# Optimization experiments

Hardware: AMD Instinct MI355X
Metric: run time of the kernel (lower is better)

Reference implementation:

```python
import jax, jax.numpy as jnp
import numpy as np

N_NODES = 50000


def _gine(x, src, dst, edge_embed, lin_w, lin_b, nn_w, nn_b):
    # PyG GINEConv (eps=0): out = nn(x + sum_{j->i} ReLU(x_j + lin(edge_attr)))
    e = edge_embed @ lin_w + lin_b              # [E, d_in]
    msg = jax.nn.relu(x[src] + e)               # gather + fuse, [E, d_in]
    agg = jax.ops.segment_sum(msg, dst, num_segments=N_NODES)  # scatter-add, [N, d_in]
    return (x + agg) @ nn_w + nn_b              # small MLP, [N, d_out]


def setup_inputs() -> dict:
    key = jax.random.key(0)
    ks = jax.random.split(key, 20)
    E = 800000
    h = 128
    sc = lambda f_in: 1.0 / np.sqrt(f_in)
    inp = {
        "x": jax.random.normal(ks[0], (N_NODES, 1), jnp.float32),
        "edge_index": jax.random.randint(ks[1], (2, E), 0, N_NODES, jnp.int64),
        "edge_attr": jax.random.normal(ks[2], (E, 1), jnp.float32),
        "em_w": jax.random.normal(ks[3], (1, h), jnp.float32) * sc(1),
        "em_b": jnp.zeros((h,), jnp.float32),
        "l1_w": jax.random.normal(ks[4], (h, 1), jnp.float32) * sc(h),
        "l1_b": jnp.zeros((1,), jnp.float32),
        "n1_w": jax.random.normal(ks[5], (1, h), jnp.float32) * sc(1),
        "n1_b": jnp.zeros((h,), jnp.float32),
        "l2_w": jax.random.normal(ks[6], (h, h), jnp.float32) * sc(h),
        "l2_b": jnp.zeros((h,), jnp.float32),
        "n2_w": jax.random.normal(ks[7], (h, h), jnp.float32) * sc(h),
        "n2_b": jnp.zeros((h,), jnp.float32),
        "l3_w": jax.random.normal(ks[8], (h, h), jnp.float32) * sc(h),
        "l3_b": jnp.zeros((h,), jnp.float32),
        "n3_w": jax.random.normal(ks[9], (h, h), jnp.float32) * sc(h),
        "n3_b": jnp.zeros((h,), jnp.float32),
        "dec_w": jax.random.normal(ks[10], (2 * h, 1), jnp.float32) * sc(2 * h),
        "dec_b": jnp.zeros((1,), jnp.float32),
    }
    return inp


def reference(x, edge_index, edge_attr, em_w, em_b, l1_w, l1_b, n1_w, n1_b,
              l2_w, l2_b, n2_w, n2_b, l3_w, l3_b, n3_w, n3_b, dec_w, dec_b):
    src, dst = edge_index[0], edge_index[1]
    edge_embed = edge_attr @ em_w + em_b                      # [E, 128]
    hdn = _gine(x,   src, dst, edge_embed, l1_w, l1_b, n1_w, n1_b)
    hdn = _gine(hdn, src, dst, edge_embed, l2_w, l2_b, n2_w, n2_b)
    hdn = _gine(hdn, src, dst, edge_embed, l3_w, l3_b, n3_w, n3_b)
    h_cat = jnp.concatenate([hdn[src], hdn[dst]], axis=-1)    # [E, 256]
    return h_cat @ dec_w + dec_b                              # [E, 1]
```

## Files before the change

kernel.cpp:

```cpp
#include <hip/hip_runtime.h>

#define H 128
#define CAPC 5376


typedef unsigned long long ull;
using bf16x8 = __attribute__((ext_vector_type(8))) short;
using f32x4  = __attribute__((ext_vector_type(4))) float;

__device__ __forceinline__ float bf2f(unsigned short v) {
  return __uint_as_float(((unsigned)v) << 16);
}
__device__ __forceinline__ unsigned short bf16r(float v) {
  unsigned u = __float_as_uint(v);
  u = (u + 0x7FFFu + ((u >> 16) & 1u)) >> 16;
  return (unsigned short)u;
}
__device__ __forceinline__ unsigned bf16pair(float a, float b) {
  return (unsigned)bf16r(a) | ((unsigned)bf16r(b) << 16);
}

__global__ __launch_bounds__(256) void init_consts(
    const float* __restrict__ em_w, const float* __restrict__ em_b,
    const float* __restrict__ l1_w, const float* __restrict__ l1_b,
    const float* __restrict__ l2_w, const float* __restrict__ l2_b,
    const float* __restrict__ n1_b,
    const float* __restrict__ l3_w, const float* __restrict__ l3_b,
    const float* __restrict__ n2w, const float* __restrict__ n3w,
    float* __restrict__ consts, int* __restrict__ cursor,
    unsigned short* __restrict__ w2t, unsigned short* __restrict__ w3t,
    int NBUCK) {
  if (blockIdx.x > 0) {
    const int i = (blockIdx.x - 1) * 256 + threadIdx.x;
    if (i < H * H) {
      const int j = i >> 7, k = i & (H - 1);
      w2t[k * H + j] = bf16r(n2w[i]);
    } else {
      const int ii = i - H * H;
      const int j = ii >> 7, k = ii & (H - 1);
      w3t[k * H + j] = bf16r(n3w[ii]);
    }
    return;
  }
  const int k = threadIdx.x;
  if (k < NBUCK) cursor[k] = 0;
  __shared__ float sa[H], sc[H];
  if (k < H) {
    float u2 = 0.f, c2 = 0.f, u3 = 0.f, c3 = 0.f;
    for (int j = 0; j < H; ++j) {
      const float ew = em_w[j], eb = em_b[j];
      u2 = fmaf(ew, l2_w[j * H + k], u2);
      c2 = fmaf(eb, l2_w[j * H + k], c2);
      u3 = fmaf(ew, l3_w[j * H + k], u3);
      c3 = fmaf(eb, l3_w[j * H + k], c3);
    }
    consts[2 + k]         = u2;
    consts[2 + H + k]     = c2 + l2_b[k] + n1_b[k];
    consts[2 + 2 * H + k] = u3;
    consts[2 + 3 * H + k] = c3 + l3_b[k];
    sa[k] = em_w[k] * l1_w[k];
    sc[k] = em_b[k] * l1_w[k];
  }
  __syncthreads();
  for (int s = 64; s > 0; s >>= 1) {
    if (k < s) { sa[k] += sa[k + s]; sc[k] += sc[k + s]; }
    __syncthreads();
  }
  if (k == 0) { consts[0] = sa[0]; consts[1] = sc[0] + l1_b[0]; }
}

__global__ __launch_bounds__(1024) void bin_scatter(
    const int* __restrict__ src, const int* __restrict__ dst,
    const float* __restrict__ ea, int* __restrict__ cursor,
    ull* __restrict__ spc, int E, int NBUCK) {
  __shared__ int lhist[256];
  __shared__ int lbase[256];
  const int tid = threadIdx.x;
  const int base = blockIdx.x * 2048 + tid * 2;
  if (tid < 256) lhist[tid] = 0;
  __syncthreads();
  int s_[2], d_[2], b_[2], r_[2];
  float a_[2];
#pragma unroll
  for (int j = 0; j < 2; ++j) {
    const int e = base + j;
    if (e < E) {
      s_[j] = src[e]; d_[j] = dst[e]; a_[j] = ea[e];
      b_[j] = d_[j] >> 8;
      r_[j] = atomicAdd(&lhist[b_[j]], 1);
    } else {
      b_[j] = -1;
    }
  }
  __syncthreads();
  if (tid < NBUCK && lhist[tid] > 0)
    lbase[tid] = atomicAdd(&cursor[tid], lhist[tid]);
  __syncthreads();
#pragma unroll
  for (int j = 0; j < 2; ++j) {
    if (b_[j] >= 0) {
      const int pl = lbase[b_[j]] + r_[j];
      if (pl < CAPC)
        spc[(size_t)b_[j] * CAPC + pl] =
            ((ull)(unsigned)(s_[j] | ((d_[j] & 255) << 16)) << 32) |
            (ull)(unsigned)__float_as_uint(a_[j]);
    }
  }
}

__global__ __launch_bounds__(1024) void fine_scatter(
    const int* __restrict__ cursor, const ull* __restrict__ spc,
    const float* __restrict__ x, const float* __restrict__ consts,
    int2* __restrict__ spf, int* __restrict__ rowstart,
    float* __restrict__ s1, int N) {
  __shared__ int lh[256];
  __shared__ int sd[256];
  __shared__ int cur[256];
  __shared__ int2 pay[CAPC];
  const int tid = threadIdx.x;
  const int b = blockIdx.x;
  const int cnt = min(cursor[b], CAPC);
  const size_t rbase = (size_t)b * CAPC;
  if (tid < 256) lh[tid] = 0;
  __syncthreads();
  for (int i = tid; i < cnt; i += 1024)
    atomicAdd(&lh[(int)((spc[rbase + i] >> 48) & 255u)], 1);
  __syncthreads();
  if (tid < 256) sd[tid] = lh[tid];
  __syncthreads();
  for (int off = 1; off < 256; off <<= 1) {
    int t = 0;
    if (tid < 256 && tid >= off) t = sd[tid - off];
    __syncthreads();
    if (tid < 256) sd[tid] += t;
    __syncthreads();
  }
  if (tid < 256) {
    const int ex = sd[tid] - lh[tid];
    cur[tid] = ex;
    rowstart[b * 257 + tid] = (int)rbase + ex;
    if (tid == 0) rowstart[b * 257 + 256] = (int)rbase + cnt;
  }
  __syncthreads();
  for (int i = tid; i < cnt; i += 1024) {
    const ull payv = spc[rbase + i];
    const int dl = (int)((payv >> 48) & 255u);
    const int pos = atomicAdd(&cur[dl], 1);
    pay[pos] = make_int2((int)((payv >> 32) & 0xFFFFu), (int)(unsigned)payv);
  }
  __syncthreads();
  for (int i = tid; i < cnt; i += 1024) spf[rbase + i] = pay[i];
  const int lane = tid & 63, wid = tid >> 6;
  const float a1 = consts[0], c1 = consts[1];
  for (int i = wid; i < 256; i += 16) {
    const int n = (b << 8) + i;
    if (n >= N) break;
    const int rsl = sd[i] - lh[i], ci = lh[i];
    float part = 0.f;
    for (int j = lane; j < ci; j += 64) {
      const int2 pv = pay[rsl + j];
      part += fmaxf(x[pv.x] + fmaf(a1, __int_as_float(pv.y), c1), 0.f);
    }
#pragma unroll
    for (int o = 32; o >= 1; o >>= 1) part += __shfl_xor(part, o, 64);
    if (lane == 0) s1[n] = x[n] + part;
  }
}

__global__ __launch_bounds__(256) void edge2_csr(
    const int* __restrict__ rowstart, const int2* __restrict__ sp,
    const float* __restrict__ s1, const float* __restrict__ n1w,
    const float* __restrict__ n1b, const float* __restrict__ consts,
    unsigned short* __restrict__ t2b, int N) {
  const int n = (blockIdx.x * blockDim.x + threadIdx.x) >> 6;
  const int lane = threadIdx.x & 63;
  if (n >= N) return;
  const int rbase = (n >> 8) * 257 + (n & 255);
  const int rs = rowstart[rbase], re = rowstart[rbase + 1];
  const float w0 = n1w[lane],            w1 = n1w[lane + 64];
  const float u0 = consts[2 + lane],     u1 = consts[2 + lane + 64];
  const float c0 = consts[2 + H + lane], c1 = consts[2 + H + lane + 64];
  float acc0 = 0.f, acc1 = 0.f;
  for (int base = rs; base < re; base += 64) {
    const int i = base + lane;
    float s1v = 0.f, eav = 0.f;
    if (i < re) {
      const int2 sv = sp[i];
      s1v = s1[sv.x];
      eav = __int_as_float(sv.y);
    }
    const int cnt = min(64, re - base);
    for (int j = 0; j < cnt; ++j) {
      const float s = __shfl(s1v, j, 64);
      const float a = __shfl(eav, j, 64);
      acc0 += fmaxf(fmaf(s, w0, fmaf(a, u0, c0)), 0.f);
      acc1 += fmaxf(fmaf(s, w1, fmaf(a, u1, c1)), 0.f);
    }
  }
  const float sn = s1[n];
  t2b[(size_t)n * H + lane]      = bf16r(fmaf(sn, w0, n1b[lane])      + acc0);
  t2b[(size_t)n * H + lane + 64] = bf16r(fmaf(sn, w1, n1b[lane + 64]) + acc1);
}

__global__ __launch_bounds__(256) void edge3_csr(
    const int* __restrict__ rowstart, const int2* __restrict__ sp,
    const unsigned short* __restrict__ h2b, const float* __restrict__ consts,
    unsigned short* __restrict__ t3b, int N) {
  const int n = (blockIdx.x * blockDim.x + threadIdx.x) >> 6;
  const int lane = threadIdx.x & 63;
  if (n >= N) return;
  const int rbase = (n >> 8) * 257 + (n & 255);
  const int rs = rowstart[rbase], re = rowstart[rbase + 1];
  const int k0 = 2 * lane;
  const float u0 = consts[2 + 2 * H + k0], u1 = consts[2 + 2 * H + k0 + 1];
  const float c0 = consts[2 + 3 * H + k0], c1 = consts[2 + 3 * H + k0 + 1];
  float acc0 = 0.f, acc1 = 0.f;
  int i = rs;
  for (; i + 4 <= re; i += 4) {
    const int2 e0 = sp[i], e1 = sp[i + 1], e2 = sp[i + 2], e3 = sp[i + 3];
    const ushort2 h0 = *(const ushort2*)&h2b[(size_t)e0.x * H + k0];
    const ushort2 h1 = *(const ushort2*)&h2b[(size_t)e1.x * H + k0];
    const ushort2 h2v = *(const ushort2*)&h2b[(size_t)e2.x * H + k0];
    const ushort2 h3 = *(const ushort2*)&h2b[(size_t)e3.x * H + k0];
    const float a0 = __int_as_float(e0.y), a1 = __int_as_float(e1.y);
    const float a2 = __int_as_float(e2.y), a3 = __int_as_float(e3.y);
    acc0 += fmaxf(bf2f(h0.x) + fmaf(a0, u0, c0), 0.f);
    acc1 += fmaxf(bf2f(h0.y) + fmaf(a0, u1, c1), 0.f);
    acc0 += fmaxf(bf2f(h1.x) + fmaf(a1, u0, c0), 0.f);
    acc1 += fmaxf(bf2f(h1.y) + fmaf(a1, u1, c1), 0.f);
    acc0 += fmaxf(bf2f(h2v.x) + fmaf(a2, u0, c0), 0.f);
    acc1 += fmaxf(bf2f(h2v.y) + fmaf(a2, u1, c1), 0.f);
    acc0 += fmaxf(bf2f(h3.x) + fmaf(a3, u0, c0), 0.f);
    acc1 += fmaxf(bf2f(h3.y) + fmaf(a3, u1, c1), 0.f);
  }
  for (; i < re; ++i) {
    const int2 ev = sp[i];
    const ushort2 hv = *(const ushort2*)&h2b[(size_t)ev.x * H + k0];
    const float a = __int_as_float(ev.y);
    acc0 += fmaxf(bf2f(hv.x) + fmaf(a, u0, c0), 0.f);
    acc1 += fmaxf(bf2f(hv.y) + fmaf(a, u1, c1), 0.f);
  }
  const ushort2 hn = *(const ushort2*)&h2b[(size_t)n * H + k0];
  ((unsigned*)t3b)[(size_t)n * 64 + lane] =
      bf16pair(bf2f(hn.x) + acc0, bf2f(hn.y) + acc1);
}

__global__ __launch_bounds__(256) void mlp2_mfma(
    const unsigned short* __restrict__ t2b, unsigned short* __restrict__ h2b,
    const unsigned short* __restrict__ w2t, const float* __restrict__ n2b,
    int N) {
  __shared__ unsigned short dt[4][16 * H];
  const int tid = threadIdx.x, w = tid >> 6, lane = tid & 63;
  const int col = lane & 15, quad = lane >> 4;
  const int tile = blockIdx.x * 4 + w;
  const int node0 = tile * 16;
  const bf16x8* arow =
      (const bf16x8*)(t2b + (size_t)(node0 + col) * H + quad * 8);
  const bf16x8 a0 = arow[0], a1 = arow[4], a2 = arow[8], a3 = arow[12];
#pragma unroll
  for (int t = 0; t < 8; ++t) {
    const bf16x8* bcol =
        (const bf16x8*)(w2t + (size_t)(t * 16 + col) * H + quad * 8);
    f32x4 acc = {0.f, 0.f, 0.f, 0.f};
    acc = __builtin_amdgcn_mfma_f32_16x16x32_bf16(a0, bcol[0], acc, 0, 0, 0);
    acc = __builtin_amdgcn_mfma_f32_16x16x32_bf16(a1, bcol[4], acc, 0, 0, 0);
    acc = __builtin_amdgcn_mfma_f32_16x16x32_bf16(a2, bcol[8], acc, 0, 0, 0);
    acc = __builtin_amdgcn_mfma_f32_16x16x32_bf16(a3, bcol[12], acc, 0, 0, 0);
    const float bias = n2b[t * 16 + col];
#pragma unroll
    for (int r = 0; r < 4; ++r)
      dt[w][(quad * 4 + r) * H + t * 16 + col] = bf16r(acc[r] + bias);
  }
  __syncthreads();
  const unsigned* du = (const unsigned*)dt;
  unsigned* gu = (unsigned*)h2b;
  const int nb = blockIdx.x * 64;
  for (int i = tid; i < 64 * 64; i += 256) {
    const int r = i >> 6;
    if (nb + r < N) gu[(size_t)(nb + r) * 64 + (i & 63)] = du[i];
  }
}

__global__ __launch_bounds__(256) void mlp3_mfma(
    const unsigned short* __restrict__ t3b, const unsigned short* __restrict__ w3t,
    const float* __restrict__ n3b, const float* __restrict__ dec_w,
    float* __restrict__ p, float* __restrict__ q, int N) {
  __shared__ float dt3[4][16 * H];
  const int tid = threadIdx.x, w = tid >> 6, lane = tid & 63;
  const int col = lane & 15, quad = lane >> 4;
  const int tile = blockIdx.x * 4 + w;
  const int node0 = tile * 16;
  const bf16x8* arow =
      (const bf16x8*)(t3b + (size_t)(node0 + col) * H + quad * 8);
  const bf16x8 a0 = arow[0], a1 = arow[4], a2 = arow[8], a3 = arow[12];
#pragma unroll
  for (int t = 0; t < 8; ++t) {
    const bf16x8* bcol =
        (const bf16x8*)(w3t + (size_t)(t * 16 + col) * H + quad * 8);
    f32x4 acc = {0.f, 0.f, 0.f, 0.f};
    acc = __builtin_amdgcn_mfma_f32_16x16x32_bf16(a0, bcol[0], acc, 0, 0, 0);
    acc = __builtin_amdgcn_mfma_f32_16x16x32_bf16(a1, bcol[4], acc, 0, 0, 0);
    acc = __builtin_amdgcn_mfma_f32_16x16x32_bf16(a2, bcol[8], acc, 0, 0, 0);
    acc = __builtin_amdgcn_mfma_f32_16x16x32_bf16(a3, bcol[12], acc, 0, 0, 0);
    const float bias = n3b[t * 16 + col];
#pragma unroll
    for (int r = 0; r < 4; ++r)
      dt3[w][(quad * 4 + r) * H + t * 16 + col] = acc[r] + bias;
  }
  __syncthreads();
  const float dwA0 = dec_w[lane], dwA1 = dec_w[64 + lane];
  const float dwB0 = dec_w[128 + lane], dwB1 = dec_w[192 + lane];
#pragma unroll 4
  for (int r = 0; r < 16; ++r) {
    const float h0 = dt3[w][r * H + lane];
    const float h1 = dt3[w][r * H + 64 + lane];
    float pd = h0 * dwA0 + h1 * dwA1;
    float qd = h0 * dwB0 + h1 * dwB1;
#pragma unroll
    for (int o = 32; o >= 1; o >>= 1) {
      pd += __shfl_xor(pd, o, 64);
      qd += __shfl_xor(qd, o, 64);
    }
    const int n = node0 + r;
    if (lane == 0 && n < N) { p[n] = pd; q[n] = qd; }
  }
}

__global__ void final_kernel(const int* __restrict__ src,
                             const int* __restrict__ dst,
                             const float* __restrict__ p,
                             const float* __restrict__ q,
                             const float* __restrict__ dec_b,
                             float* __restrict__ out, int E) {
  const int e = blockIdx.x * blockDim.x + threadIdx.x;
  if (e < E) out[e] = p[src[e]] + q[dst[e]] + dec_b[0];
}

extern "C" void kernel_launch(void* const* d_in, const int* in_sizes, int n_in,
                              void* d_out, int out_size, void* d_ws, size_t ws_size,
                              hipStream_t stream) {
  const float* x     = (const float*)d_in[0];
  const int*   ei    = (const int*)d_in[1];
  const float* ea    = (const float*)d_in[2];
  const float* em_w  = (const float*)d_in[3];
  const float* em_b  = (const float*)d_in[4];
  const float* l1_w  = (const float*)d_in[5];
  const float* l1_b  = (const float*)d_in[6];
  const float* n1_w  = (const float*)d_in[7];
  const float* n1_b  = (const float*)d_in[8];
  const float* l2_w  = (const float*)d_in[9];
  const float* l2_b  = (const float*)d_in[10];
  const float* n2_w  = (const float*)d_in[11];
  const float* n2_b  = (const float*)d_in[12];
  const float* l3_w  = (const float*)d_in[13];
  const float* l3_b  = (const float*)d_in[14];
  const float* n3_w  = (const float*)d_in[15];
  const float* n3_b  = (const float*)d_in[16];
  const float* dec_w = (const float*)d_in[17];
  const float* dec_b = (const float*)d_in[18];
  float* out = (float*)d_out;

  const int N = in_sizes[0];
  const int E = in_sizes[2];
  const int* src = ei;
  const int* dst = ei + E;

  const int NBUCK  = (N + 255) >> 8;
  const int NBATCH = (E + 2047) >> 11;
  const int NPAD   = ((N + 63) / 64) * 64;
  const int NBLK64 = NPAD / 64;

  float* ws       = (float*)d_ws;
  float* consts   = ws;
  ull*   spc      = (ull*)(ws + 1024);
  int2*  spf      = (int2*)(spc + (size_t)NBUCK * CAPC);
  unsigned short* t2b = (unsigned short*)(spf + (size_t)NBUCK * CAPC);
  unsigned short* t3b = t2b + (size_t)NPAD * H;
  unsigned short* h2b = t3b + (size_t)NPAD * H;
  unsigned short* w2t = h2b + (size_t)NPAD * H;
  unsigned short* w3t = w2t + H * H;
  float* s1       = (float*)(w3t + H * H);
  float* p        = s1 + N;
  float* q        = p + N;
  int*   cursor   = (int*)(q + N);
  int*   rowstart = cursor + 256;

  init_consts<<<129, 256, 0, stream>>>(em_w, em_b, l1_w, l1_b, l2_w, l2_b,
                                       n1_b, l3_w, l3_b, n2_w, n3_w,
                                       consts, cursor, w2t, w3t, NBUCK);
  bin_scatter<<<NBATCH, 1024, 0, stream>>>(src, dst, ea, cursor, spc, E, NBUCK);
  fine_scatter<<<NBUCK, 1024, 0, stream>>>(cursor, spc, x, consts, spf,
                                           rowstart, s1, N);

  const int nwblocks = (N + 3) / 4;
  edge2_csr<<<nwblocks, 256, 0, stream>>>(rowstart, spf, s1, n1_w, n1_b,
                                          consts, t2b, N);
  mlp2_mfma<<<NBLK64, 256, 0, stream>>>(t2b, h2b, w2t, n2_b, N);
  edge3_csr<<<nwblocks, 256, 0, stream>>>(rowstart, spf, h2b, consts, t3b, N);
  mlp3_mfma<<<NBLK64, 256, 0, stream>>>(t3b, w3t, n3_b, dec_w, p, q, N);
  final_kernel<<<(E + 255) / 256, 256, 0, stream>>>(src, dst, p, q, dec_b, out, E);
}
```

Before: 246.7 us.

## Fuse all stages into one persistent cooperative kernel with grid syncs

Replaces the eight separate kernel launches with a single cooperative kernel whose phases are separated by grid-wide syncs, using a shared-memory union across phases and grid-stride loops. It also folds the decoder dot product directly into the layer-3 MFMA epilogue via shuffles, dropping the shared staging buffer, and processes four edges per thread in the binning phase. This removes launch gaps and tail effects between stages. In exchange, occupancy is capped by the large shared-memory union and the grid size, and each phase runs on a fixed grid of at most 512 blocks.

```diff
diff --git a/kernel.cpp b/kernel.cpp
--- a/kernel.cpp
+++ b/kernel.cpp
@@ -1,4 +1,5 @@
 #include <hip/hip_runtime.h>
+#include <hip/hip_cooperative_groups.h>
 
 #define H 128
 #define CAPC 5376
@@ -7,6 +8,7 @@
 typedef unsigned long long ull;
 using bf16x8 = __attribute__((ext_vector_type(8))) short;
 using f32x4  = __attribute__((ext_vector_type(4))) float;
+namespace cg = cooperative_groups;
 
 __device__ __forceinline__ float bf2f(unsigned short v) {
   return __uint_as_float(((unsigned)v) << 16);
@@ -20,383 +22,357 @@
   return (unsigned)bf16r(a) | ((unsigned)bf16r(b) << 16);
 }
 
-__global__ __launch_bounds__(256) void init_consts(
-    const float* __restrict__ em_w, const float* __restrict__ em_b,
-    const float* __restrict__ l1_w, const float* __restrict__ l1_b,
-    const float* __restrict__ l2_w, const float* __restrict__ l2_b,
-    const float* __restrict__ n1_b,
-    const float* __restrict__ l3_w, const float* __restrict__ l3_b,
-    const float* __restrict__ n2w, const float* __restrict__ n3w,
-    float* __restrict__ consts, int* __restrict__ cursor,
-    unsigned short* __restrict__ w2t, unsigned short* __restrict__ w3t,
-    int NBUCK) {
-  if (blockIdx.x > 0) {
-    const int i = (blockIdx.x - 1) * 256 + threadIdx.x;
+struct Params {
+  const float* x; const int* src; const int* dst; const float* ea;
+  const float *em_w, *em_b, *l1_w, *l1_b, *n1_w, *n1_b, *l2_w, *l2_b,
+              *n2_w, *n2_b, *l3_w, *l3_b, *n3_w, *n3_b, *dec_w, *dec_b;
+  float* consts; ull* spc; int2* spf;
+  unsigned short *t2b, *t3b, *h2b, *w2t, *w3t;
+  float *s1, *p, *q; int *cursor, *rowstart;
+  float* out;
+  int N, E, NBUCK, NBATCH, NT16;
+};
+
+__global__ __launch_bounds__(512, 4) void fused_kernel(Params P) {
+  cg::grid_group grid = cg::this_grid();
+  __shared__ union {
+    struct { float sa[H]; float sc[H]; } c0;
+    struct { int lhist[256]; int lbase[256]; } bin;
+    struct { int lh[256]; int sd[256]; int cur[256]; int2 pay[CAPC]; } fine;
+    struct { unsigned short dt[8][16 * H]; } m2;
+  } sm;
+  const int tid = threadIdx.x;
+  const int lane = tid & 63, w = tid >> 6;
+  const int GS = gridDim.x;
+
+  for (int i = blockIdx.x * 512 + tid; i < 2 * H * H; i += GS * 512) {
     if (i < H * H) {
       const int j = i >> 7, k = i & (H - 1);
-      w2t[k * H + j] = bf16r(n2w[i]);
+      P.w2t[k * H + j] = bf16r(P.n2_w[i]);
     } else {
       const int ii = i - H * H;
       const int j = ii >> 7, k = ii & (H - 1);
-      w3t[k * H + j] = bf16r(n3w[ii]);
-    }
-    return;
-  }
-  const int k = threadIdx.x;
-  if (k < NBUCK) cursor[k] = 0;
-  __shared__ float sa[H], sc[H];
-  if (k < H) {
-    float u2 = 0.f, c2 = 0.f, u3 = 0.f, c3 = 0.f;
-    for (int j = 0; j < H; ++j) {
-      const float ew = em_w[j], eb = em_b[j];
-      u2 = fmaf(ew, l2_w[j * H + k], u2);
-      c2 = fmaf(eb, l2_w[j * H + k], c2);
-      u3 = fmaf(ew, l3_w[j * H + k], u3);
-      c3 = fmaf(eb, l3_w[j * H + k], c3);
-    }
-    consts[2 + k]         = u2;
-    consts[2 + H + k]     = c2 + l2_b[k] + n1_b[k];
-    consts[2 + 2 * H + k] = u3;
-    consts[2 + 3 * H + k] = c3 + l3_b[k];
-    sa[k] = em_w[k] * l1_w[k];
-    sc[k] = em_b[k] * l1_w[k];
-  }
-  __syncthreads();
-  for (int s = 64; s > 0; s >>= 1) {
-    if (k < s) { sa[k] += sa[k + s]; sc[k] += sc[k + s]; }
-    __syncthreads();
-  }
-  if (k == 0) { consts[0] = sa[0]; consts[1] = sc[0] + l1_b[0]; }
-}
-
-__global__ __launch_bounds__(1024) void bin_scatter(
-    const int* __restrict__ src, const int* __restrict__ dst,
-    const float* __restrict__ ea, int* __restrict__ cursor,
-    ull* __restrict__ spc, int E, int NBUCK) {
-  __shared__ int lhist[256];
-  __shared__ int lbase[256];
-  const int tid = threadIdx.x;
-  const int base = blockIdx.x * 2048 + tid * 2;
-  if (tid < 256) lhist[tid] = 0;
-  __syncthreads();
-  int s_[2], d_[2], b_[2], r_[2];
-  float a_[2];
-#pragma unroll
-  for (int j = 0; j < 2; ++j) {
-    const int e = base + j;
-    if (e < E) {
-      s_[j] = src[e]; d_[j] = dst[e]; a_[j] = ea[e];
-      b_[j] = d_[j] >> 8;
-      r_[j] = atomicAdd(&lhist[b_[j]], 1);
-    } else {
-      b_[j] = -1;
-    }
-  }
-  __syncthreads();
-  if (tid < NBUCK && lhist[tid] > 0)
-    lbase[tid] = atomicAdd(&cursor[tid], lhist[tid]);
-  __syncthreads();
-#pragma unroll
-  for (int j = 0; j < 2; ++j) {
-    if (b_[j] >= 0) {
-      const int pl = lbase[b_[j]] + r_[j];
-      if (pl < CAPC)
-        spc[(size_t)b_[j] * CAPC + pl] =
-            ((ull)(unsigned)(s_[j] | ((d_[j] & 255) << 16)) << 32) |
-            (ull)(unsigned)__float_as_uint(a_[j]);
-    }
-  }
-}
-
-__global__ __launch_bounds__(1024) void fine_scatter(
-    const int* __restrict__ cursor, const ull* __restrict__ spc,
-    const float* __restrict__ x, const float* __restrict__ consts,
-    int2* __restrict__ spf, int* __restrict__ rowstart,
-    float* __restrict__ s1, int N) {
-  __shared__ int lh[256];
-  __shared__ int sd[256];
-  __shared__ int cur[256];
-  __shared__ int2 pay[CAPC];
-  const int tid = threadIdx.x;
-  const int b = blockIdx.x;
-  const int cnt = min(cursor[b], CAPC);
-  const size_t rbase = (size_t)b * CAPC;
-  if (tid < 256) lh[tid] = 0;
-  __syncthreads();
-  for (int i = tid; i < cnt; i += 1024)
-    atomicAdd(&lh[(int)((spc[rbase + i] >> 48) & 255u)], 1);
-  __syncthreads();
-  if (tid < 256) sd[tid] = lh[tid];
-  __syncthreads();
-  for (int off = 1; off < 256; off <<= 1) {
-    int t = 0;
-    if (tid < 256 && tid >= off) t = sd[tid - off];
-    __syncthreads();
-    if (tid < 256) sd[tid] += t;
-    __syncthreads();
-  }
-  if (tid < 256) {
-    const int ex = sd[tid] - lh[tid];
-    cur[tid] = ex;
-    rowstart[b * 257 + tid] = (int)rbase + ex;
-    if (tid == 0) rowstart[b * 257 + 256] = (int)rbase + cnt;
-  }
-  __syncthreads();
-  for (int i = tid; i < cnt; i += 1024) {
-    const ull payv = spc[rbase + i];
-    const int dl = (int)((payv >> 48) & 255u);
-    const int pos = atomicAdd(&cur[dl], 1);
-    pay[pos] = make_int2((int)((payv >> 32) & 0xFFFFu), (int)(unsigned)payv);
-  }
-  __syncthreads();
-  for (int i = tid; i < cnt; i += 1024) spf[rbase + i] = pay[i];
-  const int lane = tid & 63, wid = tid >> 6;
-  const float a1 = consts[0], c1 = consts[1];
-  for (int i = wid; i < 256; i += 16) {
-    const int n = (b << 8) + i;
-    if (n >= N) break;
-    const int rsl = sd[i] - lh[i], ci = lh[i];
-    float part = 0.f;
-    for (int j = lane; j < ci; j += 64) {
-      const int2 pv = pay[rsl + j];
-      part += fmaxf(x[pv.x] + fmaf(a1, __int_as_float(pv.y), c1), 0.f);
-    }
-#pragma unroll
-    for (int o = 32; o >= 1; o >>= 1) part += __shfl_xor(part, o, 64);
-    if (lane == 0) s1[n] = x[n] + part;
-  }
-}
-
-__global__ __launch_bounds__(256) void edge2_csr(
-    const int* __restrict__ rowstart, const int2* __restrict__ sp,
-    const float* __restrict__ s1, const float* __restrict__ n1w,
-    const float* __restrict__ n1b, const float* __restrict__ consts,
-    unsigned short* __restrict__ t2b, int N) {
-  const int n = (blockIdx.x * blockDim.x + threadIdx.x) >> 6;
-  const int lane = threadIdx.x & 63;
-  if (n >= N) return;
-  const int rbase = (n >> 8) * 257 + (n & 255);
-  const int rs = rowstart[rbase], re = rowstart[rbase + 1];
-  const float w0 = n1w[lane],            w1 = n1w[lane + 64];
-  const float u0 = consts[2 + lane],     u1 = consts[2 + lane + 64];
-  const float c0 = consts[2 + H + lane], c1 = consts[2 + H + lane + 64];
-  float acc0 = 0.f, acc1 = 0.f;
-  for (int base = rs; base < re; base += 64) {
-    const int i = base + lane;
-    float s1v = 0.f, eav = 0.f;
-    if (i < re) {
-      const int2 sv = sp[i];
-      s1v = s1[sv.x];
-      eav = __int_as_float(sv.y);
-    }
-    const int cnt = min(64, re - base);
-    for (int j = 0; j < cnt; ++j) {
-      const float s = __shfl(s1v, j, 64);
-      const float a = __shfl(eav, j, 64);
-      acc0 += fmaxf(fmaf(s, w0, fmaf(a, u0, c0)), 0.f);
-      acc1 += fmaxf(fmaf(s, w1, fmaf(a, u1, c1)), 0.f);
-    }
-  }
-  const float sn = s1[n];
-  t2b[(size_t)n * H + lane]      = bf16r(fmaf(sn, w0, n1b[lane])      + acc0);
-  t2b[(size_t)n * H + lane + 64] = bf16r(fmaf(sn, w1, n1b[lane + 64]) + acc1);
-}
-
-__global__ __launch_bounds__(256) void edge3_csr(
-    const int* __restrict__ rowstart, const int2* __restrict__ sp,
-    const unsigned short* __restrict__ h2b, const float* __restrict__ consts,
-    unsigned short* __restrict__ t3b, int N) {
-  const int n = (blockIdx.x * blockDim.x + threadIdx.x) >> 6;
-  const int lane = threadIdx.x & 63;
-  if (n >= N) return;
-  const int rbase = (n >> 8) * 257 + (n & 255);
-  const int rs = rowstart[rbase], re = rowstart[rbase + 1];
-  const int k0 = 2 * lane;
-  const float u0 = consts[2 + 2 * H + k0], u1 = consts[2 + 2 * H + k0 + 1];
-  const float c0 = consts[2 + 3 * H + k0], c1 = consts[2 + 3 * H + k0 + 1];
-  float acc0 = 0.f, acc1 = 0.f;
-  int i = rs;
-  for (; i + 4 <= re; i += 4) {
-    const int2 e0 = sp[i], e1 = sp[i + 1], e2 = sp[i + 2], e3 = sp[i + 3];
-    const ushort2 h0 = *(const ushort2*)&h2b[(size_t)e0.x * H + k0];
-    const ushort2 h1 = *(const ushort2*)&h2b[(size_t)e1.x * H + k0];
-    const ushort2 h2v = *(const ushort2*)&h2b[(size_t)e2.x * H + k0];
-    const ushort2 h3 = *(const ushort2*)&h2b[(size_t)e3.x * H + k0];
-    const float a0 = __int_as_float(e0.y), a1 = __int_as_float(e1.y);
-    const float a2 = __int_as_float(e2.y), a3 = __int_as_float(e3.y);
-    acc0 += fmaxf(bf2f(h0.x) + fmaf(a0, u0, c0), 0.f);
-    acc1 += fmaxf(bf2f(h0.y) + fmaf(a0, u1, c1), 0.f);
-    acc0 += fmaxf(bf2f(h1.x) + fmaf(a1, u0, c0), 0.f);
-    acc1 += fmaxf(bf2f(h1.y) + fmaf(a1, u1, c1), 0.f);
-    acc0 += fmaxf(bf2f(h2v.x) + fmaf(a2, u0, c0), 0.f);
-    acc1 += fmaxf(bf2f(h2v.y) + fmaf(a2, u1, c1), 0.f);
-    acc0 += fmaxf(bf2f(h3.x) + fmaf(a3, u0, c0), 0.f);
-    acc1 += fmaxf(bf2f(h3.y) + fmaf(a3, u1, c1), 0.f);
-  }
-  for (; i < re; ++i) {
-    const int2 ev = sp[i];
-    const ushort2 hv = *(const ushort2*)&h2b[(size_t)ev.x * H + k0];
-    const float a = __int_as_float(ev.y);
-    acc0 += fmaxf(bf2f(hv.x) + fmaf(a, u0, c0), 0.f);
-    acc1 += fmaxf(bf2f(hv.y) + fmaf(a, u1, c1), 0.f);
-  }
-  const ushort2 hn = *(const ushort2*)&h2b[(size_t)n * H + k0];
-  ((unsigned*)t3b)[(size_t)n * 64 + lane] =
-      bf16pair(bf2f(hn.x) + acc0, bf2f(hn.y) + acc1);
-}
-
-__global__ __launch_bounds__(256) void mlp2_mfma(
-    const unsigned short* __restrict__ t2b, unsigned short* __restrict__ h2b,
-    const unsigned short* __restrict__ w2t, const float* __restrict__ n2b,
-    int N) {
-  __shared__ unsigned short dt[4][16 * H];
-  const int tid = threadIdx.x, w = tid >> 6, lane = tid & 63;
-  const int col = lane & 15, quad = lane >> 4;
-  const int tile = blockIdx.x * 4 + w;
-  const int node0 = tile * 16;
-  const bf16x8* arow =
-      (const bf16x8*)(t2b + (size_t)(node0 + col) * H + quad * 8);
-  const bf16x8 a0 = arow[0], a1 = arow[4], a2 = arow[8], a3 = arow[12];
-#pragma unroll
-  for (int t = 0; t < 8; ++t) {
-    const bf16x8* bcol =
-        (const bf16x8*)(w2t + (size_t)(t * 16 + col) * H + quad * 8);
-    f32x4 acc = {0.f, 0.f, 0.f, 0.f};
-    acc = __builtin_amdgcn_mfma_f32_16x16x32_bf16(a0, bcol[0], acc, 0, 0, 0);
-    acc = __builtin_amdgcn_mfma_f32_16x16x32_bf16(a1, bcol[4], acc, 0, 0, 0);
-    acc = __builtin_amdgcn_mfma_f32_16x16x32_bf16(a2, bcol[8], acc, 0, 0, 0);
-    acc = __builtin_amdgcn_mfma_f32_16x16x32_bf16(a3, bcol[12], acc, 0, 0, 0);
-    const float bias = n2b[t * 16 + col];
-#pragma unroll
-    for (int r = 0; r < 4; ++r)
-      dt[w][(quad * 4 + r) * H + t * 16 + col] = bf16r(acc[r] + bias);
-  }
-  __syncthreads();
-  const unsigned* du = (const unsigned*)dt;
-  unsigned* gu = (unsigned*)h2b;
-  const int nb = blockIdx.x * 64;
-  for (int i = tid; i < 64 * 64; i += 256) {
-    const int r = i >> 6;
-    if (nb + r < N) gu[(size_t)(nb + r) * 64 + (i & 63)] = du[i];
-  }
-}
-
-__global__ __launch_bounds__(256) void mlp3_mfma(
-    const unsigned short* __restrict__ t3b, const unsigned short* __restrict__ w3t,
-    const float* __restrict__ n3b, const float* __restrict__ dec_w,
-    float* __restrict__ p, float* __restrict__ q, int N) {
-  __shared__ float dt3[4][16 * H];
-  const int tid = threadIdx.x, w = tid >> 6, lane = tid & 63;
-  const int col = lane & 15, quad = lane >> 4;
-  const int tile = blockIdx.x * 4 + w;
-  const int node0 = tile * 16;
-  const bf16x8* arow =
-      (const bf16x8*)(t3b + (size_t)(node0 + col) * H + quad * 8);
-  const bf16x8 a0 = arow[0], a1 = arow[4], a2 = arow[8], a3 = arow[12];
-#pragma unroll
-  for (int t = 0; t < 8; ++t) {
-    const bf16x8* bcol =
-        (const bf16x8*)(w3t + (size_t)(t * 16 + col) * H + quad * 8);
-    f32x4 acc = {0.f, 0.f, 0.f, 0.f};
-    acc = __builtin_amdgcn_mfma_f32_16x16x32_bf16(a0, bcol[0], acc, 0, 0, 0);
-    acc = __builtin_amdgcn_mfma_f32_16x16x32_bf16(a1, bcol[4], acc, 0, 0, 0);
-    acc = __builtin_amdgcn_mfma_f32_16x16x32_bf16(a2, bcol[8], acc, 0, 0, 0);
-    acc = __builtin_amdgcn_mfma_f32_16x16x32_bf16(a3, bcol[12], acc, 0, 0, 0);
-    const float bias = n3b[t * 16 + col];
-#pragma unroll
-    for (int r = 0; r < 4; ++r)
-      dt3[w][(quad * 4 + r) * H + t * 16 + col] = acc[r] + bias;
-  }
-  __syncthreads();
-  const float dwA0 = dec_w[lane], dwA1 = dec_w[64 + lane];
-  const float dwB0 = dec_w[128 + lane], dwB1 = dec_w[192 + lane];
+      P.w3t[k * H + j] = bf16r(P.n3_w[ii]);
+    }
+  }
+  if (blockIdx.x == 0) {
+    if (tid < 256) P.cursor[tid] = 0;
+    const int k = tid;
+    if (k < H) {
+      float u2 = 0.f, c2 = 0.f, u3 = 0.f, c3 = 0.f;
+      for (int j = 0; j < H; ++j) {
+        const float ew = P.em_w[j], eb = P.em_b[j];
+        u2 = fmaf(ew, P.l2_w[j * H + k], u2);
+        c2 = fmaf(eb, P.l2_w[j * H + k], c2);
+        u3 = fmaf(ew, P.l3_w[j * H + k], u3);
+        c3 = fmaf(eb, P.l3_w[j * H + k], c3);
+      }
+      P.consts[2 + k]         = u2;
+      P.consts[2 + H + k]     = c2 + P.l2_b[k] + P.n1_b[k];
+      P.consts[2 + 2 * H + k] = u3;
+      P.consts[2 + 3 * H + k] = c3 + P.l3_b[k];
+      sm.c0.sa[k] = P.em_w[k] * P.l1_w[k];
+      sm.c0.sc[k] = P.em_b[k] * P.l1_w[k];
+    }
+    __syncthreads();
+    for (int s = 64; s > 0; s >>= 1) {
+      if (k < s) { sm.c0.sa[k] += sm.c0.sa[k + s]; sm.c0.sc[k] += sm.c0.sc[k + s]; }
+      __syncthreads();
+    }
+    if (k == 0) { P.consts[0] = sm.c0.sa[0]; P.consts[1] = sm.c0.sc[0] + P.l1_b[0]; }
+  }
+  grid.sync();
+
+  for (int bt = blockIdx.x; bt < P.NBATCH; bt += GS) {
+    __syncthreads();
+    if (tid < 256) sm.bin.lhist[tid] = 0;
+    __syncthreads();
+    const int base = bt * 2048 + tid * 4;
+    int s_[4], d_[4], b_[4], r_[4];
+    float a_[4];
+#pragma unroll
+    for (int j = 0; j < 4; ++j) {
+      const int e = base + j;
+      if (e < P.E) {
+        s_[j] = P.src[e]; d_[j] = P.dst[e]; a_[j] = P.ea[e];
+        b_[j] = d_[j] >> 8;
+        r_[j] = atomicAdd(&sm.bin.lhist[b_[j]], 1);
+      } else {
+        b_[j] = -1;
+      }
+    }
+    __syncthreads();
+    if (tid < P.NBUCK && sm.bin.lhist[tid] > 0)
+      sm.bin.lbase[tid] = atomicAdd(&P.cursor[tid], sm.bin.lhist[tid]);
+    __syncthreads();
+#pragma unroll
+    for (int j = 0; j < 4; ++j) {
+      if (b_[j] >= 0) {
+        const int pl = sm.bin.lbase[b_[j]] + r_[j];
+        if (pl < CAPC)
+          P.spc[(size_t)b_[j] * CAPC + pl] =
+              ((ull)(unsigned)(s_[j] | ((d_[j] & 255) << 16)) << 32) |
+              (ull)(unsigned)__float_as_uint(a_[j]);
+      }
+    }
+  }
+  grid.sync();
+
+  for (int b = blockIdx.x; b < P.NBUCK; b += GS) {
+    __syncthreads();
+    const int cnt = min(P.cursor[b], CAPC);
+    const size_t rbase = (size_t)b * CAPC;
+    if (tid < 256) sm.fine.lh[tid] = 0;
+    __syncthreads();
+    for (int i = tid; i < cnt; i += 512)
+      atomicAdd(&sm.fine.lh[(int)((P.spc[rbase + i] >> 48) & 255u)], 1);
+    __syncthreads();
+    if (tid < 256) sm.fine.sd[tid] = sm.fine.lh[tid];
+    __syncthreads();
+    for (int off = 1; off < 256; off <<= 1) {
+      int t = 0;
+      if (tid < 256 && tid >= off) t = sm.fine.sd[tid - off];
+      __syncthreads();
+      if (tid < 256) sm.fine.sd[tid] += t;
+      __syncthreads();
+    }
+    if (tid < 256) {
+      const int ex = sm.fine.sd[tid] - sm.fine.lh[tid];
+      sm.fine.cur[tid] = ex;
+      P.rowstart[b * 257 + tid] = (int)rbase + ex;
+      if (tid == 0) P.rowstart[b * 257 + 256] = (int)rbase + cnt;
+    }
+    __syncthreads();
+    for (int i = tid; i < cnt; i += 512) {
+      const ull payv = P.spc[rbase + i];
+      const int dl = (int)((payv >> 48) & 255u);
+      const int pos = atomicAdd(&sm.fine.cur[dl], 1);
+      sm.fine.pay[pos] = make_int2((int)((payv >> 32) & 0xFFFFu),
+                                   (int)(unsigned)payv);
+    }
+    __syncthreads();
+    for (int i = tid; i < cnt; i += 512) P.spf[rbase + i] = sm.fine.pay[i];
+    const float a1 = P.consts[0], c1 = P.consts[1];
+    for (int i = w; i < 256; i += 8) {
+      const int n = (b << 8) + i;
+      if (n >= P.N) break;
+      const int rsl = sm.fine.sd[i] - sm.fine.lh[i], ci = sm.fine.lh[i];
+      float part = 0.f;
+      for (int j = lane; j < ci; j += 64) {
+        const int2 pv = sm.fine.pay[rsl + j];
+        part += fmaxf(P.x[pv.x] + fmaf(a1, __int_as_float(pv.y), c1), 0.f);
+      }
+#pragma unroll
+      for (int o = 32; o >= 1; o >>= 1) part += __shfl_xor(part, o, 64);
+      if (lane == 0) P.s1[n] = P.x[n] + part;
+    }
+  }
+  grid.sync();
+
+  {
+    const float w0 = P.n1_w[lane],              w1 = P.n1_w[lane + 64];
+    const float u0 = P.consts[2 + lane],        u1 = P.consts[2 + lane + 64];
+    const float c0 = P.consts[2 + H + lane],    c1 = P.consts[2 + H + lane + 64];
+    const float b0 = P.n1_b[lane],              b1 = P.n1_b[lane + 64];
+    for (int n = blockIdx.x * 8 + w; n < P.N; n += GS * 8) {
+      const int rb = (n >> 8) * 257 + (n & 255);
+      const int rs = P.rowstart[rb], re = P.rowstart[rb + 1];
+      float acc0 = 0.f, acc1 = 0.f;
+      for (int base = rs; base < re; base += 64) {
+        const int i = base + lane;
+        float s1v = 0.f, eav = 0.f;
+        if (i < re) {
+          const int2 sv = P.spf[i];
+          s1v = P.s1[sv.x];
+          eav = __int_as_float(sv.y);
+        }
+        const int cntv = min(64, re - base);
+        for (int j = 0; j < cntv; ++j) {
+          const float s = __shfl(s1v, j, 64);
+          const float a = __shfl(eav, j, 64);
+          acc0 += fmaxf(fmaf(s, w0, fmaf(a, u0, c0)), 0.f);
+          acc1 += fmaxf(fmaf(s, w1, fmaf(a, u1, c1)), 0.f);
+        }
+      }
+      const float sn = P.s1[n];
+      P.t2b[(size_t)n * H + lane]      = bf16r(fmaf(sn, w0, b0) + acc0);
+      P.t2b[(size_t)n * H + lane + 64] = bf16r(fmaf(sn, w1, b1) + acc1);
+    }
+  }
+  grid.sync();
+
+  {
+    const int col = lane & 15, quad = lane >> 4;
+    for (int tile = blockIdx.x * 8 + w; tile < P.NT16; tile += GS * 8) {
+      const int node0 = tile * 16;
+      const bf16x8* arow =
+          (const bf16x8*)(P.t2b + (size_t)(node0 + col) * H + quad * 8);
+      const bf16x8 a0 = arow[0], a1 = arow[4], a2 = arow[8], a3 = arow[12];
+#pragma unroll
+      for (int t = 0; t < 8; ++t) {
+        const bf16x8* bcol =
+            (const bf16x8*)(P.w2t + (size_t)(t * 16 + col) * H + quad * 8);
+        f32x4 acc = {0.f, 0.f, 0.f, 0.f};
+        acc = __builtin_amdgcn_mfma_f32_16x16x32_bf16(a0, bcol[0], acc, 0, 0, 0);
+        acc = __builtin_amdgcn_mfma_f32_16x16x32_bf16(a1, bcol[4], acc, 0, 0, 0);
+        acc = __builtin_amdgcn_mfma_f32_16x16x32_bf16(a2, bcol[8], acc, 0, 0, 0);
+        acc = __builtin_amdgcn_mfma_f32_16x16x32_bf16(a3, bcol[12], acc, 0, 0, 0);
+        const float bias = P.n2_b[t * 16 + col];
+#pragma unroll
+        for (int r = 0; r < 4; ++r)
+          sm.m2.dt[w][(quad * 4 + r) * H + t * 16 + col] = bf16r(acc[r] + bias);
+      }
+      unsigned* gu = (unsigned*)P.h2b;
+      const unsigned* du = (const unsigned*)sm.m2.dt[w];
 #pragma unroll 4
-  for (int r = 0; r < 16; ++r) {
-    const float h0 = dt3[w][r * H + lane];
-    const float h1 = dt3[w][r * H + 64 + lane];
-    float pd = h0 * dwA0 + h1 * dwA1;
-    float qd = h0 * dwB0 + h1 * dwB1;
-#pragma unroll
-    for (int o = 32; o >= 1; o >>= 1) {
-      pd += __shfl_xor(pd, o, 64);
-      qd += __shfl_xor(qd, o, 64);
-    }
-    const int n = node0 + r;
-    if (lane == 0 && n < N) { p[n] = pd; q[n] = qd; }
-  }
-}
-
-__global__ void final_kernel(const int* __restrict__ src,
-                             const int* __restrict__ dst,
-                             const float* __restrict__ p,
-                             const float* __restrict__ q,
-                             const float* __restrict__ dec_b,
-                             float* __restrict__ out, int E) {
-  const int e = blockIdx.x * blockDim.x + threadIdx.x;
-  if (e < E) out[e] = p[src[e]] + q[dst[e]] + dec_b[0];
+      for (int r = 0; r < 16; ++r)
+        gu[(size_t)(node0 + r) * 64 + lane] = du[r * 64 + lane];
+    }
+  }
+  grid.sync();
+
+  {
+    const int k0 = 2 * lane;
+    const float u0 = P.consts[2 + 2 * H + k0], u1 = P.consts[2 + 2 * H + k0 + 1];
+    const float c0 = P.consts[2 + 3 * H + k0], c1 = P.consts[2 + 3 * H + k0 + 1];
+    for (int n = blockIdx.x * 8 + w; n < P.N; n += GS * 8) {
+      const int rb = (n >> 8) * 257 + (n & 255);
+      const int rs = P.rowstart[rb], re = P.rowstart[rb + 1];
+      float acc0 = 0.f, acc1 = 0.f;
+      int i = rs;
+      for (; i + 4 <= re; i += 4) {
+        const int2 e0 = P.spf[i], e1 = P.spf[i + 1];
+        const int2 e2 = P.spf[i + 2], e3 = P.spf[i + 3];
+        const ushort2 h0 = *(const ushort2*)&P.h2b[(size_t)e0.x * H + k0];
+        const ushort2 h1 = *(const ushort2*)&P.h2b[(size_t)e1.x * H + k0];
+        const ushort2 h2v = *(const ushort2*)&P.h2b[(size_t)e2.x * H + k0];
+        const ushort2 h3 = *(const ushort2*)&P.h2b[(size_t)e3.x * H + k0];
+        const float a0 = __int_as_float(e0.y), a1 = __int_as_float(e1.y);
+        const float a2 = __int_as_float(e2.y), a3 = __int_as_float(e3.y);
+        acc0 += fmaxf(bf2f(h0.x) + fmaf(a0, u0, c0), 0.f);
+        acc1 += fmaxf(bf2f(h0.y) + fmaf(a0, u1, c1), 0.f);
+        acc0 += fmaxf(bf2f(h1.x) + fmaf(a1, u0, c0), 0.f);
+        acc1 += fmaxf(bf2f(h1.y) + fmaf(a1, u1, c1), 0.f);
+        acc0 += fmaxf(bf2f(h2v.x) + fmaf(a2, u0, c0), 0.f);
+        acc1 += fmaxf(bf2f(h2v.y) + fmaf(a2, u1, c1), 0.f);
+        acc0 += fmaxf(bf2f(h3.x) + fmaf(a3, u0, c0), 0.f);
+        acc1 += fmaxf(bf2f(h3.y) + fmaf(a3, u1, c1), 0.f);
+      }
+      for (; i < re; ++i) {
+        const int2 ev = P.spf[i];
+        const ushort2 hv = *(const ushort2*)&P.h2b[(size_t)ev.x * H + k0];
+        const float a = __int_as_float(ev.y);
+        acc0 += fmaxf(bf2f(hv.x) + fmaf(a, u0, c0), 0.f);
+        acc1 += fmaxf(bf2f(hv.y) + fmaf(a, u1, c1), 0.f);
+      }
+      const ushort2 hn = *(const ushort2*)&P.h2b[(size_t)n * H + k0];
+      ((unsigned*)P.t3b)[(size_t)n * 64 + lane] =
+          bf16pair(bf2f(hn.x) + acc0, bf2f(hn.y) + acc1);
+    }
+  }
+  grid.sync();
+
+  {
+    const int col = lane & 15, quad = lane >> 4;
+    for (int tile = blockIdx.x * 8 + w; tile < P.NT16; tile += GS * 8) {
+      const int node0 = tile * 16;
+      const bf16x8* arow =
+          (const bf16x8*)(P.t3b + (size_t)(node0 + col) * H + quad * 8);
+      const bf16x8 a0 = arow[0], a1 = arow[4], a2 = arow[8], a3 = arow[12];
+      float pP[4] = {0.f, 0.f, 0.f, 0.f};
+      float qP[4] = {0.f, 0.f, 0.f, 0.f};
+#pragma unroll
+      for (int t = 0; t < 8; ++t) {
+        const bf16x8* bcol =
+            (const bf16x8*)(P.w3t + (size_t)(t * 16 + col) * H + quad * 8);
+        f32x4 acc = {0.f, 0.f, 0.f, 0.f};
+        acc = __builtin_amdgcn_mfma_f32_16x16x32_bf16(a0, bcol[0], acc, 0, 0, 0);
+        acc = __builtin_amdgcn_mfma_f32_16x16x32_bf16(a1, bcol[4], acc, 0, 0, 0);
+        acc = __builtin_amdgcn_mfma_f32_16x16x32_bf16(a2, bcol[8], acc, 0, 0, 0);
+        acc = __builtin_amdgcn_mfma_f32_16x16x32_bf16(a3, bcol[12], acc, 0, 0, 0);
+        const float bias = P.n3_b[t * 16 + col];
+        const float dA = P.dec_w[t * 16 + col];
+        const float dB = P.dec_w[128 + t * 16 + col];
+#pragma unroll
+        for (int r = 0; r < 4; ++r) {
+          const float h = acc[r] + bias;
+          pP[r] = fmaf(h, dA, pP[r]);
+          qP[r] = fmaf(h, dB, qP[r]);
+        }
+      }
+#pragma unroll
+      for (int o = 1; o < 16; o <<= 1) {
+#pragma unroll
+        for (int r = 0; r < 4; ++r) {
+          pP[r] += __shfl_xor(pP[r], o, 64);
+          qP[r] += __shfl_xor(qP[r], o, 64);
+        }
+      }
+      if (col == 0) {
+#pragma unroll
+        for (int r = 0; r < 4; ++r) {
+          const int n = node0 + quad * 4 + r;
+          if (n < P.N) { P.p[n] = pP[r]; P.q[n] = qP[r]; }
+        }
+      }
+    }
+  }
+  grid.sync();
+
+  {
+    const float db = P.dec_b[0];
+    for (int e = blockIdx.x * 512 + tid; e < P.E; e += GS * 512)
+      P.out[e] = P.p[P.src[e]] + P.q[P.dst[e]] + db;
+  }
 }
 
 extern "C" void kernel_launch(void* const* d_in, const int* in_sizes, int n_in,
                               void* d_out, int out_size, void* d_ws, size_t ws_size,
                               hipStream_t stream) {
-  const float* x     = (const float*)d_in[0];
-  const int*   ei    = (const int*)d_in[1];
-  const float* ea    = (const float*)d_in[2];
-  const float* em_w  = (const float*)d_in[3];
-  const float* em_b  = (const float*)d_in[4];
-  const float* l1_w  = (const float*)d_in[5];
-  const float* l1_b  = (const float*)d_in[6];
-  const float* n1_w  = (const float*)d_in[7];
-  const float* n1_b  = (const float*)d_in[8];
-  const float* l2_w  = (const float*)d_in[9];
-  const float* l2_b  = (const float*)d_in[10];
-  const float* n2_w  = (const float*)d_in[11];
-  const float* n2_b  = (const float*)d_in[12];
-  const float* l3_w  = (const float*)d_in[13];
-  const float* l3_b  = (const float*)d_in[14];
-  const float* n3_w  = (const float*)d_in[15];
-  const float* n3_b  = (const float*)d_in[16];
-  const float* dec_w = (const float*)d_in[17];
-  const float* dec_b = (const float*)d_in[18];
-  float* out = (float*)d_out;
-
   const int N = in_sizes[0];
   const int E = in_sizes[2];
-  const int* src = ei;
-  const int* dst = ei + E;
-
   const int NBUCK  = (N + 255) >> 8;
   const int NBATCH = (E + 2047) >> 11;
   const int NPAD   = ((N + 63) / 64) * 64;
-  const int NBLK64 = NPAD / 64;
-
-  float* ws       = (float*)d_ws;
-  float* consts   = ws;
-  ull*   spc      = (ull*)(ws + 1024);
-  int2*  spf      = (int2*)(spc + (size_t)NBUCK * CAPC);
-  unsigned short* t2b = (unsigned short*)(spf + (size_t)NBUCK * CAPC);
-  unsigned short* t3b = t2b + (size_t)NPAD * H;
-  unsigned short* h2b = t3b + (size_t)NPAD * H;
-  unsigned short* w2t = h2b + (size_t)NPAD * H;
-  unsigned short* w3t = w2t + H * H;
-  float* s1       = (float*)(w3t + H * H);
-  float* p        = s1 + N;
-  float* q        = p + N;
-  int*   cursor   = (int*)(q + N);
-  int*   rowstart = cursor + 256;
-
-  init_consts<<<129, 256, 0, stream>>>(em_w, em_b, l1_w, l1_b, l2_w, l2_b,
-                                       n1_b, l3_w, l3_b, n2_w, n3_w,
-                                       consts, cursor, w2t, w3t, NBUCK);
-  bin_scatter<<<NBATCH, 1024, 0, stream>>>(src, dst, ea, cursor, spc, E, NBUCK);
-  fine_scatter<<<NBUCK, 1024, 0, stream>>>(cursor, spc, x, consts, spf,
-                                           rowstart, s1, N);
-
-  const int nwblocks = (N + 3) / 4;
-  edge2_csr<<<nwblocks, 256, 0, stream>>>(rowstart, spf, s1, n1_w, n1_b,
-                                          consts, t2b, N);
-  mlp2_mfma<<<NBLK64, 256, 0, stream>>>(t2b, h2b, w2t, n2_b, N);
-  edge3_csr<<<nwblocks, 256, 0, stream>>>(rowstart, spf, h2b, consts, t3b, N);
-  mlp3_mfma<<<NBLK64, 256, 0, stream>>>(t3b, w3t, n3_b, dec_w, p, q, N);
-  final_kernel<<<(E + 255) / 256, 256, 0, stream>>>(src, dst, p, q, dec_b, out, E);
-}
+
+  Params P;
+  P.x     = (const float*)d_in[0];
+  P.src   = (const int*)d_in[1];
+  P.dst   = ((const int*)d_in[1]) + E;
+  P.ea    = (const float*)d_in[2];
+  P.em_w  = (const float*)d_in[3];  P.em_b  = (const float*)d_in[4];
+  P.l1_w  = (const float*)d_in[5];  P.l1_b  = (const float*)d_in[6];
+  P.n1_w  = (const float*)d_in[7];  P.n1_b  = (const float*)d_in[8];
+  P.l2_w  = (const float*)d_in[9];  P.l2_b  = (const float*)d_in[10];
+  P.n2_w  = (const float*)d_in[11]; P.n2_b  = (const float*)d_in[12];
+  P.l3_w  = (const float*)d_in[13]; P.l3_b  = (const float*)d_in[14];
+  P.n3_w  = (const float*)d_in[15]; P.n3_b  = (const float*)d_in[16];
+  P.dec_w = (const float*)d_in[17]; P.dec_b = (const float*)d_in[18];
+  P.out   = (float*)d_out;
+  P.N = N; P.E = E; P.NBUCK = NBUCK; P.NBATCH = NBATCH; P.NT16 = NPAD / 16;
+
+  float* ws = (float*)d_ws;
+  P.consts   = ws;
+  P.spc      = (ull*)(ws + 1024);
+  P.spf      = (int2*)(P.spc + (size_t)NBUCK * CAPC);
+  P.t2b      = (unsigned short*)(P.spf + (size_t)NBUCK * CAPC);
+  P.t3b      = P.t2b + (size_t)NPAD * H;
+  P.h2b      = P.t3b + (size_t)NPAD * H;
+  P.w2t      = P.h2b + (size_t)NPAD * H;
+  P.w3t      = P.w2t + H * H;
+  P.s1       = (float*)(P.w3t + H * H);
+  P.p        = P.s1 + N;
+  P.q        = P.p + N;
+  P.cursor   = (int*)(P.q + N);
+  P.rowstart = P.cursor + 256;
+
+  int maxB = 0;
+  hipOccupancyMaxActiveBlocksPerMultiprocessor(&maxB, fused_kernel, 512, 0);
+  if (maxB < 1) maxB = 1;
+  int grid = maxB * 256;
+  if (grid > 512) grid = 512;
+
+  void* args[] = { (void*)&P };
+  hipLaunchCooperativeKernel((void*)fused_kernel, dim3(grid), dim3(512),
+                             args, 0, stream);
+}
```

Result: slower. 560.9 us (+127.4%).
